# Kernel tuning notes

Hardware: AMD Instinct MI355X
Metric: run time of the kernel (lower is better)

Reference implementation:

```python
import jax, jax.numpy as jnp
import numpy as np

T, A = 2048, 64          # n_thread, n_agents
RAWOB, N_TP, N_GP = 120, 5, 2
E = N_TP * N_GP          # number of sub-nets (type x group placeholder)
D = RAWOB + N_TP + 1     # augmented obs dim fed to each Net
H = 128                  # hidden width of each sub-net MLP
N_ACTION = 16


def setup_inputs() -> dict:
    key = jax.random.key(0)
    ks = jax.random.split(key, 12)
    s1 = 1.0 / np.sqrt(D)
    s2 = 1.0 / np.sqrt(H)
    return {
        "obs": jax.random.normal(ks[0], (T, A, RAWOB), dtype=jnp.float32),
        "hete_pick": jax.random.randint(ks[1], (T, A), 0, E),
        "hete_type": jax.random.randint(ks[2], (T, A), 0, N_TP),
        "gp_sel_summary": jax.random.randint(ks[3], (T, N_TP), 0, N_GP),
        # per-expert actor MLP params [E, ...]
        "W1": jax.random.normal(ks[4], (E, D, H), dtype=jnp.float32) * s1,
        "b1": jnp.zeros((E, H), dtype=jnp.float32),
        "W2": jax.random.normal(ks[5], (E, H, N_ACTION), dtype=jnp.float32) * s2,
        "b2": jnp.zeros((E, N_ACTION), dtype=jnp.float32),
        # central critic params
        "Wc1": jax.random.normal(ks[6], (D, H), dtype=jnp.float32) * s1,
        "bc1": jnp.zeros((H,), dtype=jnp.float32),
        "Wc2": jax.random.normal(ks[7], (H, 1), dtype=jnp.float32) * s2,
        "bc2": jnp.zeros((1,), dtype=jnp.float32),
    }


def _augment_obs(obs, hete_type, gp_sel_summary):
    # obs <- cat(obs, hete_type, gp_sel_summary with -1 scattered at own type idx)
    t, a, _ = obs.shape
    n_tp = gp_sel_summary.shape[1]
    gp = jnp.broadcast_to(gp_sel_summary[:, None, :].astype(obs.dtype), (t, a, n_tp))
    oh = jax.nn.one_hot(hete_type, n_tp, dtype=obs.dtype)
    gp_obs = gp * (1.0 - oh) - oh  # scatter -1 at index hete_type
    return jnp.concatenate([obs, hete_type[..., None].astype(obs.dtype), gp_obs], axis=-1)


def reference(obs, hete_pick, hete_type, gp_sel_summary,
              W1, b1, W2, b2, Wc1, bc1, Wc2, bc2):
    t, a, _ = obs.shape
    x = _augment_obs(obs, hete_type, gp_sel_summary)          # [T, A, D]
    xf = x.reshape(t * a, -1)                                  # [N, D]
    pick = hete_pick.reshape(t * a)                            # [N]
    n_exp = W1.shape[0]
    # dispatch: each token routed to exactly one sub-net; dense compute + masked combine
    logits = jnp.zeros((t * a, W2.shape[-1]), dtype=obs.dtype)
    for e in range(n_exp):  # small fixed expert loop
        y = jax.nn.relu(xf @ W1[e] + b1[e]) @ W2[e] + b2[e]    # [N, n_action]
        logits = jnp.where((pick == e)[:, None], y, logits)
    logits = logits.reshape(t, a, -1)
    # central critic on all tokens
    value = (jax.nn.relu(xf @ Wc1 + bc1) @ Wc2 + bc2).reshape(t, a, 1)
    return logits, value
```

## Files before the change

### kernel.cpp

```cpp
#include <hip/hip_runtime.h>
#include <hip/hip_bf16.h>

#define T_DIM   2048
#define A_DIM   64
#define N_TOK   (T_DIM * A_DIM)
#define RAWOB   120
#define N_TP    5
#define E_EXP   10
#define D_DIM   126
#define DP      128
#define H_DIM   128
#define N_ACT   16
#define BTOK    128
#define NBLK    (N_TOK / BTOK)
#define LOGITS_SZ (N_TOK * N_ACT)

typedef __bf16 bh8 __attribute__((ext_vector_type(8)));
typedef ushort u16x8 __attribute__((ext_vector_type(8)));
typedef ushort u16x4 __attribute__((ext_vector_type(4)));
typedef short  s16x4 __attribute__((ext_vector_type(4)));
typedef float  f32x4 __attribute__((ext_vector_type(4)));

__device__ __forceinline__ f32x4 mfma16(bh8 a, bh8 b, f32x4 c) {
    return __builtin_amdgcn_mfma_f32_16x16x32_bf16(a, b, c, 0, 0, 0);
}
__device__ __forceinline__ f32x4 mfma16k16(s16x4 a, s16x4 b, f32x4 c) {
    return __builtin_amdgcn_mfma_f32_16x16x16bf16_1k(a, b, c, 0, 0, 0);
}

__device__ __forceinline__ ushort f2bf(float f) {
    unsigned x = __builtin_bit_cast(unsigned, f);
    unsigned r = (x + 0x7fffu + ((x >> 16) & 1u)) >> 16;
    return (ushort)r;
}

#define W1P_N (E_EXP * H_DIM * DP)
#define W2P_N (E_EXP * N_ACT * H_DIM)
#define WC1P_N (DP * DP)

#define PB_BLOCKS 124

__global__ __launch_bounds__(256) void prep_kernel(
    const float* __restrict__ W1, const float* __restrict__ W2,
    const float* __restrict__ Wc1, const float* __restrict__ b1,
    const float* __restrict__ bc1,
    ushort* __restrict__ W1p, ushort* __restrict__ W2p, ushort* __restrict__ Wc1p)
{
    int bx = blockIdx.x, tid = threadIdx.x;
    if (bx < 44) {
        __shared__ ushort st[32][130];
        const float* src;
        const float* bias;
        ushort* dstbase;
        int kt;
        if (bx < 40) {
            int e = bx >> 2;
            kt = bx & 3;
            src = W1 + (e * D_DIM + kt * 32) * H_DIM;
            bias = b1 + e * H_DIM;
            dstbase = W1p + e * (H_DIM * DP);
        } else {
            kt = bx - 40;
            src = Wc1 + kt * 32 * H_DIM;
            bias = bc1;
            dstbase = Wc1p;
        }
        int dmax = D_DIM - kt * 32;
#pragma unroll
        for (int p = 0; p < 16; ++p) {
            int idx = p * 256 + tid;
            int dd = idx >> 7, n = idx & 127;
            float v;
            if (dd < dmax)                    v = src[dd * H_DIM + n];
            else if (kt == 3 && dd == 30)     v = bias[n];
            else                              v = 0.f;
            st[dd][n] = f2bf(v);
        }
        __syncthreads();
#pragma unroll
        for (int p = 0; p < 16; ++p) {
            int idx = p * 256 + tid;
            int dd = idx >> 7, n = idx & 127;
            dstbase[((n >> 4) * 4 + kt) * 512 + ((dd >> 3) * 16 + (n & 15)) * 8 + (dd & 7)]
                = st[dd][n];
        }
    } else {
        int i = (bx - 44) * 256 + tid;
        int e   = i >> 11;
        int rem = i & 2047;
        int kk  = rem >> 8;
        int idx = rem & 255;
        int l = idx >> 2, j = idx & 3;
        int lq = l >> 4, lm = l & 15;
        W2p[i] = f2bf(W2[(e * H_DIM + kk * 16 + lq * 4 + j) * N_ACT + lm]);
    }
}

__global__ __launch_bounds__(512, 4) void moe_kernel(
    const float* __restrict__ obs, const int* __restrict__ pick,
    const int* __restrict__ hete_type, const int* __restrict__ gp_sel,
    const float* __restrict__ b2, const float* __restrict__ bc2,
    const ushort* __restrict__ W1p, const ushort* __restrict__ W2p,
    const ushort* __restrict__ Wc1p, const float* __restrict__ Wc2,
    float* __restrict__ out)
{
    __shared__ __align__(16) ushort xa[BTOK * 128];
    __shared__ short map[288];
    __shared__ short texp[24];
    __shared__ int lc[16], lbase[16];
    __shared__ int nt_tot;

    const int bx  = blockIdx.x;
    const int tid = threadIdx.x;
    const int gbase = bx * BTOK;

    if (tid < 16) lc[tid] = 0;
    for (int i = tid; i < 288; i += 512) map[i] = -1;
    __syncthreads();

    int mye = 0, myloc = 0;
    if (tid < BTOK) {
        mye = pick[gbase + tid];
        myloc = atomicAdd(&lc[mye], 1);
    }

#pragma unroll
    for (int p = 0; p < 4; ++p) {
        int idx = p * 512 + tid;
        if (idx < BTOK * 15) {
            int r = idx / 15, g = idx - r * 15;
            const float* s = obs + (size_t)(gbase + r) * RAWOB + g * 8;
            float4 u0 = *(const float4*)(const void*)s;
            float4 u1 = *(const float4*)(const void*)(s + 4);
            u16x8 t;
            t[0] = f2bf(u0.x); t[1] = f2bf(u0.y); t[2] = f2bf(u0.z); t[3] = f2bf(u0.w);
            t[4] = f2bf(u1.x); t[5] = f2bf(u1.y); t[6] = f2bf(u1.z); t[7] = f2bf(u1.w);
            *(u16x8*)(void*)(xa + r * 128 + (g ^ (r & 15)) * 8) = t;
        }
    }
    if (tid < BTOK) {
        int tok = gbase + tid;
        int ht = hete_type[tok];
        int tt = tok >> 6;
        u16x8 t;
        t[0] = f2bf((float)ht);
#pragma unroll
        for (int q = 0; q < N_TP; ++q) {
            float g = (q == ht) ? -1.0f : (float)gp_sel[tt * N_TP + q];
            t[1 + q] = f2bf(g);
        }
        t[6] = (ushort)0x3F80;
        t[7] = 0;
        *(u16x8*)(void*)(xa + tid * 128 + (15 ^ (tid & 15)) * 8) = t;
    }
    __syncthreads();

    if (tid == 0) {
        int pb = 0, t = 0;
#pragma unroll
        for (int e = 0; e < E_EXP; ++e) {
            lbase[e] = pb;
            int nt = (lc[e] + 15) >> 4;
            for (int k = 0; k < nt; ++k) texp[t++] = (short)e;
            pb += nt << 4;
        }
        nt_tot = t;
    }
    __syncthreads();
    if (tid < BTOK) map[lbase[mye] + myloc] = (short)tid;
    __syncthreads();

    const int w = tid >> 6;
    const int l = tid & 63;
    const int lm = l & 15;
    const int lq = l >> 4;
    const float bcv = bc2[0];

    const int NT = nt_tot;
    for (int i = w; i < NT; i += 8) {
        const int e  = texp[i];
        const int tb = i << 4;
        const int mlt = map[tb + lm];
        const int row = mlt < 0 ? 0 : mlt;
        bh8 a[4];
#pragma unroll
        for (int kt = 0; kt < 4; ++kt) {
            int g = kt * 4 + lq;
            a[kt] = *(const bh8*)(const void*)(xa + row * 128 + (g ^ (row & 15)) * 8);
        }
        const ushort* w1e = W1p + e * (H_DIM * DP);
        const ushort* w2e = W2p + e * 2048;
        const float bb = b2[e * N_ACT + lm];
        f32x4 y = (f32x4){0.f, 0.f, 0.f, 0.f};
#pragma unroll
        for (int nt = 0; nt < 8; ++nt) {
            f32x4 ae = (f32x4){0.f, 0.f, 0.f, 0.f};
#pragma unroll
            for (int kt = 0; kt < 4; ++kt) {
                bh8 wf = *(const bh8*)(const void*)(w1e + (nt * 4 + kt) * 512 + l * 8);
                ae = mfma16(wf, a[kt], ae);
            }
            u16x4 hp;
#pragma unroll
            for (int r = 0; r < 4; ++r) hp[r] = f2bf(fmaxf(ae[r], 0.f));
            s16x4 w2f = *(const s16x4*)(const void*)(w2e + nt * 256 + l * 4);
            y = mfma16k16(__builtin_bit_cast(s16x4, hp), w2f, y);
        }
#pragma unroll
        for (int r = 0; r < 4; ++r) {
            int m2 = map[tb + lq * 4 + r];
            if (m2 >= 0) out[(size_t)(gbase + m2) * N_ACT + lm] = y[r] + bb;
        }
    }

    if (w >= 4) {
        const int r0 = (w - 4) * 32;
        const int row0 = r0 + lm, row1 = r0 + 16 + lm;
        bh8 a0[4], a1[4];
#pragma unroll
        for (int kt = 0; kt < 4; ++kt) {
            int g = kt * 4 + lq;
            a0[kt] = *(const bh8*)(const void*)(xa + row0 * 128 + (g ^ (row0 & 15)) * 8);
            a1[kt] = *(const bh8*)(const void*)(xa + row1 * 128 + (g ^ (row1 & 15)) * 8);
        }
        float p0 = 0.f, p1 = 0.f;
#pragma unroll
        for (int nt = 0; nt < 8; ++nt) {
            f32x4 c0 = (f32x4){0.f,0.f,0.f,0.f}, c1 = c0;
#pragma unroll
            for (int kt = 0; kt < 4; ++kt) {
                bh8 wf = *(const bh8*)(const void*)(Wc1p + (nt * 4 + kt) * 512 + l * 8);
                c0 = mfma16(wf, a0[kt], c0);
                c1 = mfma16(wf, a1[kt], c1);
            }
            const float4 wc = *(const float4*)(const void*)(Wc2 + nt * 16 + lq * 4);
            p0 += fmaxf(c0[0], 0.f) * wc.x + fmaxf(c0[1], 0.f) * wc.y
                + fmaxf(c0[2], 0.f) * wc.z + fmaxf(c0[3], 0.f) * wc.w;
            p1 += fmaxf(c1[0], 0.f) * wc.x + fmaxf(c1[1], 0.f) * wc.y
                + fmaxf(c1[2], 0.f) * wc.z + fmaxf(c1[3], 0.f) * wc.w;
        }
        p0 += __shfl_xor(p0, 16, 64); p0 += __shfl_xor(p0, 32, 64);
        p1 += __shfl_xor(p1, 16, 64); p1 += __shfl_xor(p1, 32, 64);
        if (lq == 0) {
            out[LOGITS_SZ + gbase + row0] = p0 + bcv;
            out[LOGITS_SZ + gbase + row1] = p1 + bcv;
        }
    }
}

extern "C" void kernel_launch(void* const* d_in, const int* in_sizes, int n_in,
                              void* d_out, int out_size, void* d_ws, size_t ws_size,
                              hipStream_t stream) {
    const float* obs  = (const float*)d_in[0];
    const int*   pick = (const int*)d_in[1];
    const int*   htyp = (const int*)d_in[2];
    const int*   gp   = (const int*)d_in[3];
    const float* W1   = (const float*)d_in[4];
    const float* b1   = (const float*)d_in[5];
    const float* W2   = (const float*)d_in[6];
    const float* b2   = (const float*)d_in[7];
    const float* Wc1  = (const float*)d_in[8];
    const float* bc1  = (const float*)d_in[9];
    const float* Wc2  = (const float*)d_in[10];
    const float* bc2  = (const float*)d_in[11];
    float* out = (float*)d_out;

    ushort* W1p  = (ushort*)d_ws;
    ushort* W2p  = W1p + W1P_N;
    ushort* Wc1p = W2p + W2P_N;

    prep_kernel<<<PB_BLOCKS, 256, 0, stream>>>(
        W1, W2, Wc1, b1, bc1, W1p, W2p, Wc1p);
    moe_kernel<<<NBLK, 512, 0, stream>>>(
        obs, pick, htyp, gp, b2, bc2,
        W1p, W2p, Wc1p, Wc2, out);
}
```

Baseline: 144.6 us.

## Process expert token tiles in pairs and double block token count

```diff
diff --git a/kernel.cpp b/kernel.cpp
--- a/kernel.cpp
+++ b/kernel.cpp
@@ -11,7 +11,7 @@
 #define DP      128
 #define H_DIM   128
 #define N_ACT   16
-#define BTOK    128
+#define BTOK    256
 #define NBLK    (N_TOK / BTOK)
 #define LOGITS_SZ (N_TOK * N_ACT)
 
@@ -105,17 +105,18 @@
     float* __restrict__ out)
 {
     __shared__ __align__(16) ushort xa[BTOK * 128];
-    __shared__ short map[288];
-    __shared__ short texp[24];
+    __shared__ short map[576];
+    __shared__ short jexp[24];
+    __shared__ short jtb[24];
     __shared__ int lc[16], lbase[16];
-    __shared__ int nt_tot;
+    __shared__ int nj_tot;
 
     const int bx  = blockIdx.x;
     const int tid = threadIdx.x;
     const int gbase = bx * BTOK;
 
     if (tid < 16) lc[tid] = 0;
-    for (int i = tid; i < 288; i += 512) map[i] = -1;
+    for (int i = tid; i < 576; i += 512) map[i] = -1;
     __syncthreads();
 
     int mye = 0, myloc = 0;
@@ -125,7 +126,7 @@
     }
 
 #pragma unroll
-    for (int p = 0; p < 4; ++p) {
+    for (int p = 0; p < 8; ++p) {
         int idx = p * 512 + tid;
         if (idx < BTOK * 15) {
             int r = idx / 15, g = idx - r * 15;
@@ -156,15 +157,20 @@
     __syncthreads();
 
     if (tid == 0) {
-        int pb = 0, t = 0;
+        int pb = 0, nj = 0;
 #pragma unroll
         for (int e = 0; e < E_EXP; ++e) {
             lbase[e] = pb;
-            int nt = (lc[e] + 15) >> 4;
-            for (int k = 0; k < nt; ++k) texp[t++] = (short)e;
-            pb += nt << 4;
-        }
-        nt_tot = t;
+            int ntile = (lc[e] + 15) >> 4;
+            int npair = (ntile + 1) >> 1;
+            for (int k = 0; k < npair; ++k) {
+                jexp[nj] = (short)e;
+                jtb[nj]  = (short)(pb + k * 32);
+                ++nj;
+            }
+            pb += npair * 32;
+        }
+        nj_tot = nj;
     }
     __syncthreads();
     if (tid < BTOK) map[lbase[mye] + myloc] = (short)tid;
@@ -176,45 +182,56 @@
     const int lq = l >> 4;
     const float bcv = bc2[0];
 
-    const int NT = nt_tot;
-    for (int i = w; i < NT; i += 8) {
-        const int e  = texp[i];
-        const int tb = i << 4;
-        const int mlt = map[tb + lm];
-        const int row = mlt < 0 ? 0 : mlt;
-        bh8 a[4];
+    const int NJ = nj_tot;
+    for (int i = w; i < NJ; i += 8) {
+        const int e  = jexp[i];
+        const int tb = jtb[i];
+        const int m0 = map[tb + lm];
+        const int m1 = map[tb + 16 + lm];
+        const int row0 = m0 < 0 ? 0 : m0;
+        const int row1 = m1 < 0 ? 0 : m1;
+        bh8 a0[4], a1[4];
 #pragma unroll
         for (int kt = 0; kt < 4; ++kt) {
             int g = kt * 4 + lq;
-            a[kt] = *(const bh8*)(const void*)(xa + row * 128 + (g ^ (row & 15)) * 8);
+            a0[kt] = *(const bh8*)(const void*)(xa + row0 * 128 + (g ^ (row0 & 15)) * 8);
+            a1[kt] = *(const bh8*)(const void*)(xa + row1 * 128 + (g ^ (row1 & 15)) * 8);
         }
         const ushort* w1e = W1p + e * (H_DIM * DP);
         const ushort* w2e = W2p + e * 2048;
         const float bb = b2[e * N_ACT + lm];
-        f32x4 y = (f32x4){0.f, 0.f, 0.f, 0.f};
+        f32x4 y0 = (f32x4){0.f, 0.f, 0.f, 0.f};
+        f32x4 y1 = (f32x4){0.f, 0.f, 0.f, 0.f};
 #pragma unroll
         for (int nt = 0; nt < 8; ++nt) {
-            f32x4 ae = (f32x4){0.f, 0.f, 0.f, 0.f};
+            f32x4 ae0 = (f32x4){0.f, 0.f, 0.f, 0.f}, ae1 = ae0;
 #pragma unroll
             for (int kt = 0; kt < 4; ++kt) {
                 bh8 wf = *(const bh8*)(const void*)(w1e + (nt * 4 + kt) * 512 + l * 8);
-                ae = mfma16(wf, a[kt], ae);
-            }
-            u16x4 hp;
-#pragma unroll
-            for (int r = 0; r < 4; ++r) hp[r] = f2bf(fmaxf(ae[r], 0.f));
+                ae0 = mfma16(wf, a0[kt], ae0);
+                ae1 = mfma16(wf, a1[kt], ae1);
+            }
+            u16x4 hp0, hp1;
+#pragma unroll
+            for (int r = 0; r < 4; ++r) {
+                hp0[r] = f2bf(fmaxf(ae0[r], 0.f));
+                hp1[r] = f2bf(fmaxf(ae1[r], 0.f));
+            }
             s16x4 w2f = *(const s16x4*)(const void*)(w2e + nt * 256 + l * 4);
-            y = mfma16k16(__builtin_bit_cast(s16x4, hp), w2f, y);
+            y0 = mfma16k16(__builtin_bit_cast(s16x4, hp0), w2f, y0);
+            y1 = mfma16k16(__builtin_bit_cast(s16x4, hp1), w2f, y1);
         }
 #pragma unroll
         for (int r = 0; r < 4; ++r) {
-            int m2 = map[tb + lq * 4 + r];
-            if (m2 >= 0) out[(size_t)(gbase + m2) * N_ACT + lm] = y[r] + bb;
-        }
-    }
-
-    if (w >= 4) {
-        const int r0 = (w - 4) * 32;
+            int s0 = map[tb + lq * 4 + r];
+            if (s0 >= 0) out[(size_t)(gbase + s0) * N_ACT + lm] = y0[r] + bb;
+            int s1 = map[tb + 16 + lq * 4 + r];
+            if (s1 >= 0) out[(size_t)(gbase + s1) * N_ACT + lm] = y1[r] + bb;
+        }
+    }
+
+    {
+        const int r0 = w * 32;
         const int row0 = r0 + lm, row1 = r0 + 16 + lm;
         bh8 a0[4], a1[4];
 #pragma unroll
```

New measurement: 131.6 us, median of 2. 9.0% less time.
